# Optimization experiments

Hardware: AMD Instinct MI355X
Metric: run time of the kernel (lower is better)

Reference implementation:

```python
import jax, jax.numpy as jnp
import numpy as np

DIM = 512
N_HEAD = 4
WIN = (5, 9)

def setup_inputs() -> dict:
    key = jax.random.key(0)
    ks = jax.random.split(key, 9)
    s = DIM ** -0.5
    x = jax.random.normal(ks[0], (1, 8, 60, 108, DIM), jnp.float32)
    Wq = jax.random.normal(ks[1], (DIM, DIM), jnp.float32) * s
    bq = jax.random.normal(ks[2], (DIM,), jnp.float32) * 0.02
    Wk = jax.random.normal(ks[3], (DIM, DIM), jnp.float32) * s
    bk = jax.random.normal(ks[4], (DIM,), jnp.float32) * 0.02
    Wv = jax.random.normal(ks[5], (DIM, DIM), jnp.float32) * s
    bv = jax.random.normal(ks[6], (DIM,), jnp.float32) * 0.02
    Wp = jax.random.normal(ks[7], (DIM, DIM), jnp.float32) * s
    bp = jax.random.normal(ks[8], (DIM,), jnp.float32) * 0.02
    return {"x": x, "Wq": Wq, "bq": bq, "Wk": Wk, "bk": bk,
            "Wv": Wv, "bv": bv, "Wp": Wp, "bp": bp}

def reference(x, Wq, bq, Wk, bk, Wv, bv, Wp, bp):
    b, t, h, w, c = x.shape
    w_h, w_w = WIN
    n_head = N_HEAD
    c_head = c // n_head
    n_wh = -(-h // w_h)
    n_ww = -(-w // w_w)
    new_h, new_w = n_wh * w_h, n_ww * w_w
    pad_b, pad_r = new_h - h, new_w - w
    if pad_b > 0 or pad_r > 0:
        x = jnp.pad(x, ((0, 0), (0, 0), (0, pad_b), (0, pad_r), (0, 0)))
    # torch nn.Linear: y = x @ W.T + b, weight shape (out, in)
    q = jnp.einsum('bthwc,dc->bthwd', x, Wq) + bq
    k = jnp.einsum('bthwc,dc->bthwd', x, Wk) + bk
    v = jnp.einsum('bthwc,dc->bthwd', x, Wv) + bv

    def part(z):
        # (b,t,H,W,c) -> (b, n_windows, n_head, t*w_h*w_w, c_head)
        z = z.reshape(b, t, n_wh, w_h, n_ww, w_w, n_head, c_head)
        z = z.transpose(0, 2, 4, 6, 1, 3, 5, 7)
        return z.reshape(b, n_wh * n_ww, n_head, t * w_h * w_w, c_head)

    qw, kw, vw = part(q), part(k), part(v)
    scale = c_head ** -0.5
    # all (batch, window) attentions batched into one einsum (fused form of the torch double loop)
    scores = jnp.einsum('bwnsc,bwnkc->bwnsk', qw, kw) * scale
    attn = jax.nn.softmax(scores, axis=-1)
    out = jnp.einsum('bwnsk,bwnkc->bwnsc', attn, vw)
    # merge windows back: (b,t,new_h,new_w,c)
    out = out.reshape(b, n_wh, n_ww, n_head, t, w_h, w_w, c_head)
    out = out.transpose(0, 4, 1, 5, 2, 6, 3, 7).reshape(b, t, new_h, new_w, c)
    out = out[:, :, :h, :w, :]
    out = jnp.einsum('bthwc,dc->bthwd', out, Wp) + bp
    return out
```

## Files before the change

kernel.cpp:

```cpp
#include <hip/hip_runtime.h>

typedef _Float16 f16;
typedef _Float16 f16x8 __attribute__((ext_vector_type(8)));
typedef _Float16 f16x4 __attribute__((ext_vector_type(4)));
typedef float f32x4 __attribute__((ext_vector_type(4)));
typedef unsigned int u32;
typedef unsigned int u32x4 __attribute__((ext_vector_type(4)));

#define MFMA16(a, b, c) __builtin_amdgcn_mfma_f32_16x16x32_f16(a, b, c, 0, 0, 0)

__device__ __forceinline__ void async_copy16(f16* lds, const f16* g) {
    __builtin_amdgcn_global_load_lds(
        (const __attribute__((address_space(1))) unsigned int*)g,
        (__attribute__((address_space(3))) unsigned int*)lds,
        16, 0, 0);
}

__global__ __launch_bounds__(256) void prep_kernel(
    const float* __restrict__ Wq, const float* __restrict__ Wk,
    const float* __restrict__ Wv, const float* __restrict__ Wp,
    const float* __restrict__ bq, const float* __restrict__ bk,
    const float* __restrict__ bv,
    f16* __restrict__ Wqkv, f16* __restrict__ Wph, float* __restrict__ bqkv,
    int* __restrict__ tokmap)
{
    int i = blockIdx.x * 256 + threadIdx.x;
    if (i < 786432) {
        int r = i >> 9, c = i & 511;
        const float* src = (r < 512) ? Wq : (r < 1024) ? Wk : Wv;
        Wqkv[i] = (f16)src[(r & 511) * 512 + c];
    } else if (i < 786432 + 262144) {
        int j = i - 786432;
        Wph[j] = (f16)Wp[j];
    } else if (i < 786432 + 262144 + 1536) {
        int j = i - (786432 + 262144);
        bqkv[j] = (j < 512) ? bq[j] : (j < 1024) ? bk[j - 512] : bv[j - 1024];
    } else if (i < 786432 + 262144 + 1536 + 51840) {
        int j = i - (786432 + 262144 + 1536);
        int t_ = j / 6480, rem = j % 6480;
        int hh = rem / 108, ww = rem % 108;
        int win = (hh / 5) * 12 + (ww / 9);
        int s = t_ * 45 + (hh % 5) * 9 + (ww % 9);
        tokmap[j] = win * 1440 + s;
    }
}

__global__ __launch_bounds__(256) void convert_x(
    const float* __restrict__ x, f16* __restrict__ xh)
{
    int i = blockIdx.x * 256 + threadIdx.x;
    f32x4 a = *(const f32x4*)(x + (size_t)i * 8);
    f32x4 b = *(const f32x4*)(x + (size_t)i * 8 + 4);
    f16x8 h = { (f16)a[0], (f16)a[1], (f16)a[2], (f16)a[3],
                (f16)b[0], (f16)b[1], (f16)b[2], (f16)b[3] };
    *(f16x8*)(xh + (size_t)i * 8) = h;
}

__global__ __launch_bounds__(256) void qkv_gemm(
    const f16* __restrict__ Xh, const f16* __restrict__ W,
    const float* __restrict__ bias, const int* __restrict__ tokmap,
    f16* __restrict__ Qp, f16* __restrict__ Kp, f16* __restrict__ Vp)
{
    __shared__ __align__(16) f16 As[2][128 * 64];
    __shared__ __align__(16) f16 Bs[2][128 * 64];
    const int tid = threadIdx.x;
    const int lane = tid & 63, wid = tid >> 6;
    const int g = lane >> 4, l15 = lane & 15;
    const int wr = wid >> 1, wc = wid & 1;

    const int orig = blockIdx.x;
    const int xcd = orig & 7;
    const int wg = (xcd < 4 ? xcd * 608 : 2432 + (xcd - 4) * 607) + (orig >> 3);
    const int bn = wg % 12;
    const int brow = (wg / 12) * 128;

    const f16* Abase = Xh + (size_t)brow * 512;
    const f16* Bbase = W + (size_t)bn * 128 * 512;

    f32x4 acc[4][4] = {};

    #define QKV_STAGE(buf, step)                                              \
        {                                                                     \
            const int k0_ = (step) * 64;                                      \
            _Pragma("unroll")                                                 \
            for (int rr = 0; rr < 4; ++rr) {                                  \
                int idx = rr * 256 + tid;                                     \
                int row = idx >> 3, ch = idx & 7;                             \
                int sch = ch ^ (row & 7);                                     \
                async_copy16(&As[buf][idx * 8],                               \
                             Abase + (size_t)row * 512 + k0_ + sch * 8);      \
                async_copy16(&Bs[buf][idx * 8],                               \
                             Bbase + (size_t)row * 512 + k0_ + sch * 8);      \
            }                                                                 \
        }

    QKV_STAGE(0, 0);
    asm volatile("s_waitcnt vmcnt(0)" ::: "memory");
    __syncthreads();

    int cur = 0;
    for (int step = 0; step < 8; ++step) {
        if (step < 7) QKV_STAGE(cur ^ 1, step + 1);
        #pragma unroll
        for (int kk = 0; kk < 2; ++kk) {
            f16x8 a[4], b[4];
            #pragma unroll
            for (int m = 0; m < 4; ++m) {
                int arow = wr * 64 + m * 16 + l15;
                int acol = (kk * 4 + g) ^ (arow & 7);
                a[m] = *(const f16x8*)&As[cur][arow * 64 + acol * 8];
            }
            #pragma unroll
            for (int n = 0; n < 4; ++n) {
                int brow_ = wc * 64 + n * 16 + l15;
                int bcol = (kk * 4 + g) ^ (brow_ & 7);
                b[n] = *(const f16x8*)&Bs[cur][brow_ * 64 + bcol * 8];
            }
            #pragma unroll
            for (int m = 0; m < 4; ++m)
                #pragma unroll
                for (int n = 0; n < 4; ++n)
                    acc[m][n] = MFMA16(a[m], b[n], acc[m][n]);
        }
        asm volatile("s_waitcnt vmcnt(0)" ::: "memory");
        __syncthreads();
        cur ^= 1;
    }
    #undef QKV_STAGE

    const int which = bn >> 2, head = bn & 3;
    f16* dst = (which == 0) ? Qp : (which == 1) ? Kp : Vp;
    #pragma unroll
    for (int m = 0; m < 4; ++m) {
        #pragma unroll
        for (int j = 0; j < 4; ++j) {
            int gm = brow + wr * 64 + m * 16 + g * 4 + j;
            size_t obase = ((size_t)(tokmap[gm] + head * 360)) * 128;
            #pragma unroll
            for (int n = 0; n < 4; ++n) {
                int cidx = wc * 64 + n * 16 + l15;
                float v = acc[m][n][j] + bias[bn * 128 + cidx];
                dst[obase + cidx] = (f16)v;
            }
        }
    }
}

__global__ __launch_bounds__(256, 2) void attn_kernel(
    const f16* __restrict__ Qp, const f16* __restrict__ Kp,
    const f16* __restrict__ Vp, f16* __restrict__ AO)
{
    __shared__ __align__(16) f16 Kl[64 * 136];
    __shared__ __align__(16) f16 Vt[128 * 72];
    __shared__ __align__(16) f16 Pl[192 * 72];

    const int tid = threadIdx.x;
    const int lane = tid & 63, wid = tid >> 6;
    const int g = lane >> 4, l15 = lane & 15;
    const int wh = blockIdx.x >> 1;
    const int half = blockIdx.x & 1;
    const int win = wh >> 2, head = wh & 3;
    const int base = wh * 46080;
    const int qbase = half * 192 + wid * 48;

    const float SC2 = 0.08838834764831845f * 1.4426950408889634f;

    f16x8 qf[3][4];
    #pragma unroll
    for (int qi = 0; qi < 3; ++qi)
        #pragma unroll
        for (int c4 = 0; c4 < 4; ++c4)
            qf[qi][c4] = *(const f16x8*)(Qp + base + (qbase + qi * 16 + l15) * 128 + c4 * 32 + g * 8);

    f32x4 o[3][8] = {};
    float m_r[3] = { -1e30f, -1e30f, -1e30f };
    float l_r[3] = { 0.f, 0.f, 0.f };

    for (int kt = 0; kt < 6; ++kt) {
        #pragma unroll
        for (int it = 0; it < 4; ++it) {
            int idx = it * 256 + tid;
            int krow = idx >> 4, seg = idx & 15;
            f16x8 kv = *(const f16x8*)(Kp + base + (kt * 64 + krow) * 128 + seg * 8);
            *(f16x8*)&Kl[krow * 136 + seg * 8] = kv;
        }
        #pragma unroll
        for (int it = 0; it < 2; ++it) {
            int i2 = it * 256 + tid;
            int kb = i2 >> 6;
            int chp = (i2 & 63) * 2;
            const u32* Vb = (const u32*)(Vp + base);
            u32 d[8];
            #pragma unroll
            for (int i = 0; i < 8; ++i) {
                int kg = kt * 64 + kb * 8 + i;
                d[i] = (kg < 360) ? Vb[kg * 64 + (chp >> 1)] : 0u;
            }
            u32x4 lo, hi;
            #pragma unroll
            for (int jj = 0; jj < 4; ++jj) {
                lo[jj] = (d[2 * jj] & 0xffffu) | (d[2 * jj + 1] << 16);
                hi[jj] = (d[2 * jj] >> 16) | (d[2 * jj + 1] & 0xffff0000u);
            }
            *(u32x4*)&Vt[chp * 72 + kb * 8] = lo;
            *(u32x4*)&Vt[(chp + 1) * 72 + kb * 8] = hi;
        }
        __syncthreads();

        f32x4 sc[4][3] = {};
        __builtin_amdgcn_s_setprio(1);
        #pragma unroll
        for (int c4 = 0; c4 < 4; ++c4) {
            f16x8 ka[4];
            #pragma unroll
            for (int kf = 0; kf < 4; ++kf)
                ka[kf] = *(const f16x8*)&Kl[(kf * 16 + l15) * 136 + c4 * 32 + g * 8];
            #pragma unroll
            for (int kf = 0; kf < 4; ++kf)
                #pragma unroll
                for (int qi = 0; qi < 3; ++qi)
                    sc[kf][qi] = MFMA16(ka[kf], qf[qi][c4], sc[kf][qi]);
        }
        __builtin_amdgcn_s_setprio(0);
        if (kt == 5) {
            #pragma unroll
            for (int kf = 0; kf < 4; ++kf)
                #pragma unroll
                for (int j = 0; j < 4; ++j)
                    if (320 + kf * 16 + g * 4 + j >= 360) {
                        #pragma unroll
                        for (int qi = 0; qi < 3; ++qi) sc[kf][qi][j] = -1e30f;
                    }
        }

        #pragma unroll
        for (int qi = 0; qi < 3; ++qi) {
            float mx = -1e30f;
            #pragma unroll
            for (int kf = 0; kf < 4; ++kf)
                #pragma unroll
                for (int j = 0; j < 4; ++j)
                    mx = fmaxf(mx, sc[kf][qi][j]);
            mx = fmaxf(mx, __shfl_xor(mx, 16));
            mx = fmaxf(mx, __shfl_xor(mx, 32));
            float mnew = fmaxf(m_r[qi], mx);
            float r = exp2f((m_r[qi] - mnew) * SC2);
            m_r[qi] = mnew;
            float psum = 0.f;
            #pragma unroll
            for (int kf = 0; kf < 4; ++kf) {
                f16x4 pv;
                #pragma unroll
                for (int j = 0; j < 4; ++j) {
                    float p = exp2f((sc[kf][qi][j] - mnew) * SC2);
                    psum += p;
                    pv[j] = (f16)p;
                }
                *(f16x4*)&Pl[(wid * 48 + qi * 16 + l15) * 72 + kf * 16 + g * 4] = pv;
            }
            psum += __shfl_xor(psum, 16);
            psum += __shfl_xor(psum, 32);
            l_r[qi] = l_r[qi] * r + psum;
            #pragma unroll
            for (int j = 0; j < 4; ++j) {
                float rj = __shfl(r, g * 4 + j);
                #pragma unroll
                for (int chf = 0; chf < 8; ++chf)
                    o[qi][chf][j] *= rj;
            }
        }

        __builtin_amdgcn_s_setprio(1);
        #pragma unroll
        for (int kc = 0; kc < 2; ++kc) {
            f16x8 pa[3], vb[8];
            #pragma unroll
            for (int qi = 0; qi < 3; ++qi)
                pa[qi] = *(const f16x8*)&Pl[(wid * 48 + qi * 16 + l15) * 72 + kc * 32 + g * 8];
            #pragma unroll
            for (int chf = 0; chf < 8; ++chf)
                vb[chf] = *(const f16x8*)&Vt[(chf * 16 + l15) * 72 + kc * 32 + g * 8];
            #pragma unroll
            for (int qi = 0; qi < 3; ++qi)
                #pragma unroll
                for (int chf = 0; chf < 8; ++chf)
                    o[qi][chf] = MFMA16(pa[qi], vb[chf], o[qi][chf]);
        }
        __builtin_amdgcn_s_setprio(0);
        __syncthreads();
    }

    #pragma unroll
    for (int qi = 0; qi < 3; ++qi) {
        #pragma unroll
        for (int j = 0; j < 4; ++j) {
            float lj = __shfl(l_r[qi], g * 4 + j);
            float inv = 1.0f / lj;
            int s = qbase + qi * 16 + g * 4 + j;
            if (s < 360) {
                int t_ = s / 45, s45 = s % 45;
                int hh = (win / 12) * 5 + s45 / 9;
                int ww = (win % 12) * 9 + s45 % 9;
                int mm = t_ * 6480 + hh * 108 + ww;
                #pragma unroll
                for (int chf = 0; chf < 8; ++chf) {
                    int col = head * 128 + chf * 16 + l15;
                    AO[(size_t)mm * 512 + col] = (f16)(o[qi][chf][j] * inv);
                }
            }
        }
    }
}

__global__ __launch_bounds__(256) void proj_gemm(
    const f16* __restrict__ A, const f16* __restrict__ W,
    const float* __restrict__ bias, float* __restrict__ out)
{
    __shared__ __align__(16) f16 As[2][128 * 64];
    __shared__ __align__(16) f16 Bs[2][128 * 64];
    const int tid = threadIdx.x;
    const int lane = tid & 63, wid = tid >> 6;
    const int g = lane >> 4, l15 = lane & 15;
    const int wr = wid >> 1, wc = wid & 1;

    const int orig = blockIdx.x;
    const int xcd = orig & 7;
    const int wg = (xcd < 4 ? xcd * 203 : 812 + (xcd - 4) * 202) + (orig >> 3);
    const int bcol = (wg & 3) * 128;
    const int brow = (wg >> 2) * 128;

    const f16* Abase = A + (size_t)brow * 512;
    const f16* Bbase = W + (size_t)bcol * 512;

    f32x4 acc[4][4] = {};

    #define PROJ_STAGE(buf, step)                                             \
        {                                                                     \
            const int k0_ = (step) * 64;                                      \
            _Pragma("unroll")                                                 \
            for (int rr = 0; rr < 4; ++rr) {                                  \
                int idx = rr * 256 + tid;                                     \
                int row = idx >> 3, ch = idx & 7;                             \
                int sch = ch ^ (row & 7);                                     \
                async_copy16(&As[buf][idx * 8],                               \
                             Abase + (size_t)row * 512 + k0_ + sch * 8);      \
                async_copy16(&Bs[buf][idx * 8],                               \
                             Bbase + (size_t)row * 512 + k0_ + sch * 8);      \
            }                                                                 \
        }

    PROJ_STAGE(0, 0);
    asm volatile("s_waitcnt vmcnt(0)" ::: "memory");
    __syncthreads();

    int cur = 0;
    for (int step = 0; step < 8; ++step) {
        if (step < 7) PROJ_STAGE(cur ^ 1, step + 1);
        #pragma unroll
        for (int kk = 0; kk < 2; ++kk) {
            f16x8 a[4], b[4];
            #pragma unroll
            for (int m = 0; m < 4; ++m) {
                int arow = wr * 64 + m * 16 + l15;
                int acol = (kk * 4 + g) ^ (arow & 7);
                a[m] = *(const f16x8*)&As[cur][arow * 64 + acol * 8];
            }
            #pragma unroll
            for (int n = 0; n < 4; ++n) {
                int brow_ = wc * 64 + n * 16 + l15;
                int bcol_ = (kk * 4 + g) ^ (brow_ & 7);
                b[n] = *(const f16x8*)&Bs[cur][brow_ * 64 + bcol_ * 8];
            }
            #pragma unroll
            for (int m = 0; m < 4; ++m)
                #pragma unroll
                for (int n = 0; n < 4; ++n)
                    acc[m][n] = MFMA16(a[m], b[n], acc[m][n]);
        }
        asm volatile("s_waitcnt vmcnt(0)" ::: "memory");
        __syncthreads();
        cur ^= 1;
    }
    #undef PROJ_STAGE

    #pragma unroll
    for (int m = 0; m < 4; ++m)
        #pragma unroll
        for (int j = 0; j < 4; ++j) {
            int gm = brow + wr * 64 + m * 16 + g * 4 + j;
            #pragma unroll
            for (int n = 0; n < 4; ++n) {
                int gn = bcol + wc * 64 + n * 16 + l15;
                out[(size_t)gm * 512 + gn] = acc[m][n][j] + bias[gn];
            }
        }
}

extern "C" void kernel_launch(void* const* d_in, const int* in_sizes, int n_in,
                              void* d_out, int out_size, void* d_ws, size_t ws_size,
                              hipStream_t stream)
{
    (void)in_sizes; (void)n_in; (void)out_size; (void)ws_size;
    const float* x  = (const float*)d_in[0];
    const float* Wq = (const float*)d_in[1];
    const float* bq = (const float*)d_in[2];
    const float* Wk = (const float*)d_in[3];
    const float* bk = (const float*)d_in[4];
    const float* Wv = (const float*)d_in[5];
    const float* bv = (const float*)d_in[6];
    const float* Wp = (const float*)d_in[7];
    const float* bp = (const float*)d_in[8];

    f16* Qp   = (f16*)d_ws;
    f16* Kp   = Qp + 26542080;
    f16* Vp   = Kp + 26542080;
    f16* AO   = Vp + 26542080;
    f16* xh   = AO;
    f16* Wqkv = AO + 26542080;
    f16* Wph  = Wqkv + 786432;
    float* bqkv = (float*)(Wph + 262144);
    int* tokmap = (int*)(bqkv + 1536);

    prep_kernel<<<4305, 256, 0, stream>>>(Wq, Wk, Wv, Wp, bq, bk, bv, Wqkv, Wph, bqkv, tokmap);
    convert_x<<<12960, 256, 0, stream>>>(x, xh);
    qkv_gemm<<<4860, 256, 0, stream>>>(xh, Wqkv, bqkv, tokmap, Qp, Kp, Vp);
    attn_kernel<<<1152, 256, 0, stream>>>(Qp, Kp, Vp, AO);
    proj_gemm<<<1620, 256, 0, stream>>>(AO, Wph, bp, (float*)d_out);
}
```

Measured before the change: 291.9 us.

## Restructure QKV GEMM into 256x256 tiles with 8-wave interleaved load/MFMA pipeline

The QKV projection GEMM now uses 256x256 output tiles with 512 threads (8 waves), down from 128x128 tiles with 256 threads. Each wave computes a 128x64 sub-tile. The K-loop is split into four quarter phases that interleave LDS fragment reads, async global-to-LDS stage loads and MFMA bursts. These phases are separated by barriers and raised wave priority during MFMA. The larger tile raises arithmetic intensity and cuts redundant global loads of X and W, but it uses roughly 128KB of LDS per block and needs a row bound check for the partial last tile.

```diff
diff --git a/kernel.cpp b/kernel.cpp
--- a/kernel.cpp
+++ b/kernel.cpp
@@ -56,91 +56,161 @@
     *(f16x8*)(xh + (size_t)i * 8) = h;
 }
 
-__global__ __launch_bounds__(256) void qkv_gemm(
+__global__ __launch_bounds__(512, 2) void qkv_gemm(
     const f16* __restrict__ Xh, const f16* __restrict__ W,
     const float* __restrict__ bias, const int* __restrict__ tokmap,
     f16* __restrict__ Qp, f16* __restrict__ Kp, f16* __restrict__ Vp)
 {
-    __shared__ __align__(16) f16 As[2][128 * 64];
-    __shared__ __align__(16) f16 Bs[2][128 * 64];
+    __shared__ __align__(16) f16 As[2][2][128 * 64];
+    __shared__ __align__(16) f16 Bs[2][2][128 * 64];
     const int tid = threadIdx.x;
-    const int lane = tid & 63, wid = tid >> 6;
+    const int lane = tid & 63;
+    const int wid = tid >> 6;
     const int g = lane >> 4, l15 = lane & 15;
-    const int wr = wid >> 1, wc = wid & 1;
+    const int wr = wid >> 2;
+    const int wc = wid & 3;
 
     const int orig = blockIdx.x;
     const int xcd = orig & 7;
-    const int wg = (xcd < 4 ? xcd * 608 : 2432 + (xcd - 4) * 607) + (orig >> 3);
-    const int bn = wg % 12;
-    const int brow = (wg / 12) * 128;
+    const int wg = (xcd < 2 ? xcd * 153 : 306 + (xcd - 2) * 152) + (orig >> 3);
+    const int bn = wg % 6;
+    const int bm = wg / 6;
+    const int brow = bm * 256;
 
     const f16* Abase = Xh + (size_t)brow * 512;
-    const f16* Bbase = W + (size_t)bn * 128 * 512;
-
-    f32x4 acc[4][4] = {};
-
-    #define QKV_STAGE(buf, step)                                              \
-        {                                                                     \
-            const int k0_ = (step) * 64;                                      \
-            _Pragma("unroll")                                                 \
-            for (int rr = 0; rr < 4; ++rr) {                                  \
-                int idx = rr * 256 + tid;                                     \
-                int row = idx >> 3, ch = idx & 7;                             \
-                int sch = ch ^ (row & 7);                                     \
-                async_copy16(&As[buf][idx * 8],                               \
-                             Abase + (size_t)row * 512 + k0_ + sch * 8);      \
-                async_copy16(&Bs[buf][idx * 8],                               \
-                             Bbase + (size_t)row * 512 + k0_ + sch * 8);      \
-            }                                                                 \
-        }
-
-    QKV_STAGE(0, 0);
-    asm volatile("s_waitcnt vmcnt(0)" ::: "memory");
-    __syncthreads();
-
-    int cur = 0;
-    for (int step = 0; step < 8; ++step) {
-        if (step < 7) QKV_STAGE(cur ^ 1, step + 1);
-        #pragma unroll
-        for (int kk = 0; kk < 2; ++kk) {
-            f16x8 a[4], b[4];
-            #pragma unroll
-            for (int m = 0; m < 4; ++m) {
-                int arow = wr * 64 + m * 16 + l15;
-                int acol = (kk * 4 + g) ^ (arow & 7);
-                a[m] = *(const f16x8*)&As[cur][arow * 64 + acol * 8];
-            }
-            #pragma unroll
-            for (int n = 0; n < 4; ++n) {
-                int brow_ = wc * 64 + n * 16 + l15;
-                int bcol = (kk * 4 + g) ^ (brow_ & 7);
-                b[n] = *(const f16x8*)&Bs[cur][brow_ * 64 + bcol * 8];
-            }
-            #pragma unroll
-            for (int m = 0; m < 4; ++m)
-                #pragma unroll
-                for (int n = 0; n < 4; ++n)
-                    acc[m][n] = MFMA16(a[m], b[n], acc[m][n]);
-        }
-        asm volatile("s_waitcnt vmcnt(0)" ::: "memory");
-        __syncthreads();
-        cur ^= 1;
-    }
-    #undef QKV_STAGE
-
-    const int which = bn >> 2, head = bn & 3;
+    const f16* Bbase = W + (size_t)bn * 256 * 512;
+
+    auto stage_op = [&](int op, int t) {
+        const int p = t & 1;
+        const int h = op & 1;
+        const int k0 = t * 64;
+        const f16* src = (op < 2) ? Abase : Bbase;
+        f16* dst = (op < 2) ? &As[p][h][0] : &Bs[p][h][0];
+        #pragma unroll
+        for (int i = 0; i < 2; ++i) {
+            int idx = i * 512 + tid;
+            int row = idx >> 3, ch = idx & 7;
+            int sch = ch ^ (row & 7);
+            async_copy16(dst + idx * 8,
+                         src + (size_t)(h * 128 + row) * 512 + k0 + sch * 8);
+        }
+    };
+
+    f32x4 acc[8][4] = {};
+    f16x8 ar[4][2], br[4][2];
+
+    stage_op(0, 0); stage_op(1, 0); stage_op(2, 0); stage_op(3, 0);
+    stage_op(0, 1);
+    asm volatile("s_waitcnt vmcnt(2)" ::: "memory");
+    __builtin_amdgcn_s_barrier();
+
+    for (int t = 0; t < 8; ++t) {
+        const int p = t & 1;
+        #pragma unroll
+        for (int mf = 0; mf < 4; ++mf)
+            #pragma unroll
+            for (int kk = 0; kk < 2; ++kk) {
+                int row = mf * 16 + l15;
+                int sl = (kk * 4 + g) ^ (row & 7);
+                ar[mf][kk] = *(const f16x8*)&As[p][wr][row * 64 + sl * 8];
+            }
+        #pragma unroll
+        for (int nf = 0; nf < 2; ++nf)
+            #pragma unroll
+            for (int kk = 0; kk < 2; ++kk) {
+                int rn = (wc & 1) * 64 + nf * 16 + l15;
+                int sl = (kk * 4 + g) ^ (rn & 7);
+                br[nf][kk] = *(const f16x8*)&Bs[p][wc >> 1][rn * 64 + sl * 8];
+            }
+        if (t + 1 < 8) stage_op(1, t + 1);
+        __builtin_amdgcn_s_barrier();
+        __builtin_amdgcn_s_setprio(1);
+        #pragma unroll
+        for (int m = 0; m < 4; ++m)
+            #pragma unroll
+            for (int n = 0; n < 2; ++n)
+                #pragma unroll
+                for (int kk = 0; kk < 2; ++kk)
+                    acc[m][n] = MFMA16(ar[m][kk], br[n][kk], acc[m][n]);
+        __builtin_amdgcn_s_setprio(0);
+        __builtin_amdgcn_s_barrier();
+
+        #pragma unroll
+        for (int nf = 2; nf < 4; ++nf)
+            #pragma unroll
+            for (int kk = 0; kk < 2; ++kk) {
+                int rn = (wc & 1) * 64 + nf * 16 + l15;
+                int sl = (kk * 4 + g) ^ (rn & 7);
+                br[nf][kk] = *(const f16x8*)&Bs[p][wc >> 1][rn * 64 + sl * 8];
+            }
+        if (t + 1 < 8) stage_op(2, t + 1);
+        __builtin_amdgcn_s_barrier();
+        __builtin_amdgcn_s_setprio(1);
+        #pragma unroll
+        for (int m = 0; m < 4; ++m)
+            #pragma unroll
+            for (int n = 2; n < 4; ++n)
+                #pragma unroll
+                for (int kk = 0; kk < 2; ++kk)
+                    acc[m][n] = MFMA16(ar[m][kk], br[n][kk], acc[m][n]);
+        __builtin_amdgcn_s_setprio(0);
+        __builtin_amdgcn_s_barrier();
+
+        #pragma unroll
+        for (int mf = 0; mf < 4; ++mf)
+            #pragma unroll
+            for (int kk = 0; kk < 2; ++kk) {
+                int row = 64 + mf * 16 + l15;
+                int sl = (kk * 4 + g) ^ (row & 7);
+                ar[mf][kk] = *(const f16x8*)&As[p][wr][row * 64 + sl * 8];
+            }
+        if (t + 1 < 8) stage_op(3, t + 1);
+        __builtin_amdgcn_s_barrier();
+        __builtin_amdgcn_s_setprio(1);
+        #pragma unroll
+        for (int m = 0; m < 4; ++m)
+            #pragma unroll
+            for (int n = 2; n < 4; ++n)
+                #pragma unroll
+                for (int kk = 0; kk < 2; ++kk)
+                    acc[4 + m][n] = MFMA16(ar[m][kk], br[n][kk], acc[4 + m][n]);
+        __builtin_amdgcn_s_setprio(0);
+        __builtin_amdgcn_s_barrier();
+
+        if (t + 2 < 8) stage_op(0, t + 2);
+        __builtin_amdgcn_s_setprio(1);
+        #pragma unroll
+        for (int m = 0; m < 4; ++m)
+            #pragma unroll
+            for (int n = 0; n < 2; ++n)
+                #pragma unroll
+                for (int kk = 0; kk < 2; ++kk)
+                    acc[4 + m][n] = MFMA16(ar[m][kk], br[n][kk], acc[4 + m][n]);
+        __builtin_amdgcn_s_setprio(0);
+        if (t < 7) {
+            if (t + 2 < 8) asm volatile("s_waitcnt vmcnt(2)" ::: "memory");
+            else           asm volatile("s_waitcnt vmcnt(0)" ::: "memory");
+        }
+        __builtin_amdgcn_s_barrier();
+    }
+
+    const int gc0 = bn * 256 + wc * 64;
+    const int which = gc0 >> 9;
+    const int head = (gc0 >> 7) & 3;
     f16* dst = (which == 0) ? Qp : (which == 1) ? Kp : Vp;
     #pragma unroll
-    for (int m = 0; m < 4; ++m) {
+    for (int m = 0; m < 8; ++m) {
         #pragma unroll
         for (int j = 0; j < 4; ++j) {
-            int gm = brow + wr * 64 + m * 16 + g * 4 + j;
-            size_t obase = ((size_t)(tokmap[gm] + head * 360)) * 128;
-            #pragma unroll
-            for (int n = 0; n < 4; ++n) {
-                int cidx = wc * 64 + n * 16 + l15;
-                float v = acc[m][n][j] + bias[bn * 128 + cidx];
-                dst[obase + cidx] = (f16)v;
+            int gm = brow + wr * 128 + m * 16 + g * 4 + j;
+            if (gm < 51840) {
+                size_t obase = ((size_t)(tokmap[gm] + head * 360)) * 128;
+                #pragma unroll
+                for (int n = 0; n < 4; ++n) {
+                    int gcol = gc0 + n * 16 + l15;
+                    float v = acc[m][n][j] + bias[gcol];
+                    dst[obase + (gcol & 127)] = (f16)v;
+                }
             }
         }
     }
@@ -423,7 +493,7 @@
 
     prep_kernel<<<4305, 256, 0, stream>>>(Wq, Wk, Wv, Wp, bq, bk, bv, Wqkv, Wph, bqkv, tokmap);
     convert_x<<<12960, 256, 0, stream>>>(x, xh);
-    qkv_gemm<<<4860, 256, 0, stream>>>(xh, Wqkv, bqkv, tokmap, Qp, Kp, Vp);
+    qkv_gemm<<<1218, 512, 0, stream>>>(xh, Wqkv, bqkv, tokmap, Qp, Kp, Vp);
     attn_kernel<<<1152, 256, 0, stream>>>(Qp, Kp, Vp, AO);
     proj_gemm<<<1620, 256, 0, stream>>>(AO, Wph, bp, (float*)d_out);
 }
```

Result: no change. 297.5 us (+1.9%).

## Use three-stage BK=32 async pipeline with partial vmcnt waits in GEMMs

Applied to the files above, without the earlier changes.

Both the QKV and projection GEMMs move from a double-buffered K=64 tile loop to a triple-buffered K=32 loop, keeping two stages of global-to-LDS loads in flight. Each step waits with a partial vmcnt instead of a full drain. The XOR swizzle is rewritten for the narrower rows, and s_setprio is raised around the MFMA block. LDS use drops from 64KB to 48KB per block, and launch bounds request 3 blocks per CU to raise occupancy. In exchange, each iteration runs more barriers for less compute.

```diff
diff --git a/kernel.cpp b/kernel.cpp
--- a/kernel.cpp
+++ b/kernel.cpp
@@ -56,13 +56,13 @@
     *(f16x8*)(xh + (size_t)i * 8) = h;
 }
 
-__global__ __launch_bounds__(256) void qkv_gemm(
+__global__ __launch_bounds__(256, 3) void qkv_gemm(
     const f16* __restrict__ Xh, const f16* __restrict__ W,
     const float* __restrict__ bias, const int* __restrict__ tokmap,
     f16* __restrict__ Qp, f16* __restrict__ Kp, f16* __restrict__ Vp)
 {
-    __shared__ __align__(16) f16 As[2][128 * 64];
-    __shared__ __align__(16) f16 Bs[2][128 * 64];
+    __shared__ __align__(16) f16 As[3][128 * 32];
+    __shared__ __align__(16) f16 Bs[3][128 * 32];
     const int tid = threadIdx.x;
     const int lane = tid & 63, wid = tid >> 6;
     const int g = lane >> 4, l15 = lane & 15;
@@ -81,12 +81,12 @@
 
     #define QKV_STAGE(buf, step)                                              \
         {                                                                     \
-            const int k0_ = (step) * 64;                                      \
+            const int k0_ = (step) * 32;                                      \
             _Pragma("unroll")                                                 \
-            for (int rr = 0; rr < 4; ++rr) {                                  \
+            for (int rr = 0; rr < 2; ++rr) {                                  \
                 int idx = rr * 256 + tid;                                     \
-                int row = idx >> 3, ch = idx & 7;                             \
-                int sch = ch ^ (row & 7);                                     \
+                int row = idx >> 2, ch = idx & 3;                             \
+                int sch = ch ^ ((row >> 1) & 3);                              \
                 async_copy16(&As[buf][idx * 8],                               \
                              Abase + (size_t)row * 512 + k0_ + sch * 8);      \
                 async_copy16(&Bs[buf][idx * 8],                               \
@@ -95,36 +95,40 @@
         }
 
     QKV_STAGE(0, 0);
-    asm volatile("s_waitcnt vmcnt(0)" ::: "memory");
-    __syncthreads();
+    QKV_STAGE(1, 1);
 
     int cur = 0;
-    for (int step = 0; step < 8; ++step) {
-        if (step < 7) QKV_STAGE(cur ^ 1, step + 1);
-        #pragma unroll
-        for (int kk = 0; kk < 2; ++kk) {
-            f16x8 a[4], b[4];
-            #pragma unroll
-            for (int m = 0; m < 4; ++m) {
-                int arow = wr * 64 + m * 16 + l15;
-                int acol = (kk * 4 + g) ^ (arow & 7);
-                a[m] = *(const f16x8*)&As[cur][arow * 64 + acol * 8];
-            }
-            #pragma unroll
-            for (int n = 0; n < 4; ++n) {
-                int brow_ = wc * 64 + n * 16 + l15;
-                int bcol = (kk * 4 + g) ^ (brow_ & 7);
-                b[n] = *(const f16x8*)&Bs[cur][brow_ * 64 + bcol * 8];
-            }
-            #pragma unroll
-            for (int m = 0; m < 4; ++m)
-                #pragma unroll
-                for (int n = 0; n < 4; ++n)
-                    acc[m][n] = MFMA16(a[m], b[n], acc[m][n]);
-        }
-        asm volatile("s_waitcnt vmcnt(0)" ::: "memory");
-        __syncthreads();
-        cur ^= 1;
+    for (int t = 0; t < 16; ++t) {
+        if (t < 15) asm volatile("s_waitcnt vmcnt(4)" ::: "memory");
+        else        asm volatile("s_waitcnt vmcnt(0)" ::: "memory");
+        __builtin_amdgcn_s_barrier();
+        __builtin_amdgcn_sched_barrier(0);
+        if (t + 2 < 16) {
+            int stg = cur + 2; if (stg >= 3) stg -= 3;
+            QKV_STAGE(stg, t + 2);
+        }
+        f16x8 a[4], b[4];
+        #pragma unroll
+        for (int m = 0; m < 4; ++m) {
+            int arow = wr * 64 + m * 16 + l15;
+            int sl = g ^ ((arow >> 1) & 3);
+            a[m] = *(const f16x8*)&As[cur][arow * 32 + sl * 8];
+        }
+        #pragma unroll
+        for (int n = 0; n < 4; ++n) {
+            int brw = wc * 64 + n * 16 + l15;
+            int sl = g ^ ((brw >> 1) & 3);
+            b[n] = *(const f16x8*)&Bs[cur][brw * 32 + sl * 8];
+        }
+        __builtin_amdgcn_s_setprio(1);
+        #pragma unroll
+        for (int m = 0; m < 4; ++m)
+            #pragma unroll
+            for (int n = 0; n < 4; ++n)
+                acc[m][n] = MFMA16(a[m], b[n], acc[m][n]);
+        __builtin_amdgcn_s_setprio(0);
+        __builtin_amdgcn_s_barrier();
+        cur = (cur == 2) ? 0 : cur + 1;
     }
     #undef QKV_STAGE
 
@@ -312,12 +316,12 @@
     }
 }
 
-__global__ __launch_bounds__(256) void proj_gemm(
+__global__ __launch_bounds__(256, 3) void proj_gemm(
     const f16* __restrict__ A, const f16* __restrict__ W,
     const float* __restrict__ bias, float* __restrict__ out)
 {
-    __shared__ __align__(16) f16 As[2][128 * 64];
-    __shared__ __align__(16) f16 Bs[2][128 * 64];
+    __shared__ __align__(16) f16 As[3][128 * 32];
+    __shared__ __align__(16) f16 Bs[3][128 * 32];
     const int tid = threadIdx.x;
     const int lane = tid & 63, wid = tid >> 6;
     const int g = lane >> 4, l15 = lane & 15;
@@ -336,12 +340,12 @@
 
     #define PROJ_STAGE(buf, step)                                             \
         {                                                                     \
-            const int k0_ = (step) * 64;                                      \
+            const int k0_ = (step) * 32;                                      \
             _Pragma("unroll")                                                 \
-            for (int rr = 0; rr < 4; ++rr) {                                  \
+            for (int rr = 0; rr < 2; ++rr) {                                  \
                 int idx = rr * 256 + tid;                                     \
-                int row = idx >> 3, ch = idx & 7;                             \
-                int sch = ch ^ (row & 7);                                     \
+                int row = idx >> 2, ch = idx & 3;                             \
+                int sch = ch ^ ((row >> 1) & 3);                              \
                 async_copy16(&As[buf][idx * 8],                               \
                              Abase + (size_t)row * 512 + k0_ + sch * 8);      \
                 async_copy16(&Bs[buf][idx * 8],                               \
@@ -350,36 +354,40 @@
         }
 
     PROJ_STAGE(0, 0);
-    asm volatile("s_waitcnt vmcnt(0)" ::: "memory");
-    __syncthreads();
+    PROJ_STAGE(1, 1);
 
     int cur = 0;
-    for (int step = 0; step < 8; ++step) {
-        if (step < 7) PROJ_STAGE(cur ^ 1, step + 1);
-        #pragma unroll
-        for (int kk = 0; kk < 2; ++kk) {
-            f16x8 a[4], b[4];
-            #pragma unroll
-            for (int m = 0; m < 4; ++m) {
-                int arow = wr * 64 + m * 16 + l15;
-                int acol = (kk * 4 + g) ^ (arow & 7);
-                a[m] = *(const f16x8*)&As[cur][arow * 64 + acol * 8];
-            }
-            #pragma unroll
-            for (int n = 0; n < 4; ++n) {
-                int brow_ = wc * 64 + n * 16 + l15;
-                int bcol_ = (kk * 4 + g) ^ (brow_ & 7);
-                b[n] = *(const f16x8*)&Bs[cur][brow_ * 64 + bcol_ * 8];
-            }
-            #pragma unroll
-            for (int m = 0; m < 4; ++m)
-                #pragma unroll
-                for (int n = 0; n < 4; ++n)
-                    acc[m][n] = MFMA16(a[m], b[n], acc[m][n]);
-        }
-        asm volatile("s_waitcnt vmcnt(0)" ::: "memory");
-        __syncthreads();
-        cur ^= 1;
+    for (int t = 0; t < 16; ++t) {
+        if (t < 15) asm volatile("s_waitcnt vmcnt(4)" ::: "memory");
+        else        asm volatile("s_waitcnt vmcnt(0)" ::: "memory");
+        __builtin_amdgcn_s_barrier();
+        __builtin_amdgcn_sched_barrier(0);
+        if (t + 2 < 16) {
+            int stg = cur + 2; if (stg >= 3) stg -= 3;
+            PROJ_STAGE(stg, t + 2);
+        }
+        f16x8 a[4], b[4];
+        #pragma unroll
+        for (int m = 0; m < 4; ++m) {
+            int arow = wr * 64 + m * 16 + l15;
+            int sl = g ^ ((arow >> 1) & 3);
+            a[m] = *(const f16x8*)&As[cur][arow * 32 + sl * 8];
+        }
+        #pragma unroll
+        for (int n = 0; n < 4; ++n) {
+            int brw = wc * 64 + n * 16 + l15;
+            int sl = g ^ ((brw >> 1) & 3);
+            b[n] = *(const f16x8*)&Bs[cur][brw * 32 + sl * 8];
+        }
+        __builtin_amdgcn_s_setprio(1);
+        #pragma unroll
+        for (int m = 0; m < 4; ++m)
+            #pragma unroll
+            for (int n = 0; n < 4; ++n)
+                acc[m][n] = MFMA16(a[m], b[n], acc[m][n]);
+        __builtin_amdgcn_s_setprio(0);
+        __builtin_amdgcn_s_barrier();
+        cur = (cur == 2) ? 0 : cur + 1;
     }
     #undef PROJ_STAGE
 
```

New measurement: 288.3 us. About the same (-1.2%).
